# Kernel tuning notes

Hardware: AMD Instinct MI355X
Metric: run time of the kernel (lower is better)

## Reference

```python
import jax, jax.numpy as jnp
import numpy as np
import math

DIM = 768
HEADS = 12
HEAD_DIM = DIM // HEADS


def setup_inputs() -> dict:
    key = jax.random.key(0)
    ks = jax.random.split(key, 9)
    s = 1.0 / math.sqrt(DIM)
    x = jax.random.normal(ks[0], (8, 4096, DIM), dtype=jnp.float32)
    Wq = jax.random.normal(ks[1], (DIM, DIM), dtype=jnp.float32) * s
    bq = jnp.zeros((DIM,), dtype=jnp.float32)
    Wk = jax.random.normal(ks[2], (DIM, DIM), dtype=jnp.float32) * s
    bk = jnp.zeros((DIM,), dtype=jnp.float32)
    Wv = jax.random.normal(ks[3], (DIM, DIM), dtype=jnp.float32) * s
    bv = jnp.zeros((DIM,), dtype=jnp.float32)
    Wp = jax.random.normal(ks[4], (DIM, DIM), dtype=jnp.float32) * s
    bp = jnp.zeros((DIM,), dtype=jnp.float32)
    return {"x": x, "Wq": Wq, "bq": bq, "Wk": Wk, "bk": bk,
            "Wv": Wv, "bv": bv, "Wp": Wp, "bp": bp}


def reference(x, Wq, bq, Wk, bk, Wv, bv, Wp, bp):
    B, N, C = x.shape
    H, D = HEADS, HEAD_DIM
    # torch Linear: y = x @ W.T + b
    q = (x @ Wq.T + bq).reshape(B, N, H, D).transpose(0, 2, 1, 3)  # [B,H,N,D]
    k = (x @ Wk.T + bk).reshape(B, N, H, D).transpose(0, 2, 1, 3)
    v = (x @ Wv.T + bv).reshape(B, N, H, D).transpose(0, 2, 1, 3)
    q = jax.nn.softmax(q, axis=-1)   # softmax over head_dim
    k = jax.nn.softmax(k, axis=-2)   # softmax over sequence
    kv = jnp.einsum('bhnd,bhne->bhde', k, v) / math.sqrt(D)  # [B,H,D,D]
    out = jnp.einsum('bhnd,bhde->bhne', q, kv)               # [B,H,N,D]
    out = out.transpose(0, 2, 1, 3).reshape(B, N, C)
    return out @ Wp.T + bp
```

## Files before the change

kernel.cpp:

```cpp
#include <hip/hip_runtime.h>
#include <hip/hip_bf16.h>


#define AS1 __attribute__((address_space(1)))
#define AS3 __attribute__((address_space(3)))

typedef __attribute__((ext_vector_type(8))) short    s16x8;
typedef __attribute__((ext_vector_type(4))) float    f32x4;
typedef __attribute__((ext_vector_type(8))) _Float16 f16x8;
typedef __attribute__((ext_vector_type(4))) unsigned short u16x4;

__device__ __forceinline__ unsigned short f2bf(float f) {
  union { float f; unsigned u; } v; v.f = f;
  unsigned r = v.u + 0x7FFFu + ((v.u >> 16) & 1u);
  return (unsigned short)(r >> 16);
}

__global__ __launch_bounds__(256) void prep(const float* __restrict__ x,
                                            const float* __restrict__ Wq, const float* __restrict__ Wk,
                                            const float* __restrict__ Wv,
                                            const float* __restrict__ bq, const float* __restrict__ bk,
                                            const float* __restrict__ bv,
                                            unsigned short* __restrict__ x_bf,
                                            unsigned short* __restrict__ wqkv_bf,
                                            float* __restrict__ bqkv) {
  const int XB = 2304;
  if ((int)blockIdx.x >= XB) {
    int j = (blockIdx.x - XB) * 256 + threadIdx.x;
    if (j < 768) bqkv[j] = bq[j];
    else if (j < 1536) bqkv[j] = bk[j - 768];
    else if (j < 2304) bqkv[j] = bv[j - 1536];
    return;
  }
  const int n8x = 3145728, n8w = 73728;
  const int stride = XB * 256;
  for (int i = blockIdx.x * 256 + threadIdx.x; i < n8x + 3 * n8w; i += stride) {
    const float* s; unsigned short* d;
    if (i < n8x) { s = x + (size_t)i * 8; d = x_bf + (size_t)i * 8; }
    else {
      int wi = i - n8x, w = wi / n8w, off = wi - w * n8w;
      const float* ws_ = (w == 0) ? Wq : (w == 1) ? Wk : Wv;
      s = ws_ + (size_t)off * 8; d = wqkv_bf + (size_t)wi * 8;
    }
    f32x4 a = ((const f32x4*)s)[0], b = ((const f32x4*)s)[1];
    u16x4 lo, hi;
    lo[0] = f2bf(a[0]); lo[1] = f2bf(a[1]); lo[2] = f2bf(a[2]); lo[3] = f2bf(a[3]);
    hi[0] = f2bf(b[0]); hi[1] = f2bf(b[1]); hi[2] = f2bf(b[2]); hi[3] = f2bf(b[3]);
    ((u16x4*)d)[0] = lo; ((u16x4*)d)[1] = hi;
  }
}

template <int MODE>
__global__ __launch_bounds__(256, 3) void gemm128(const unsigned short* __restrict__ A,
                                                  const unsigned short* __restrict__ Bm,
                                                  const float* __restrict__ bias,
                                                  void* out0, void* out1, void* out2,
                                                  int N, int K, int nb, int batchedB) {
  __shared__ unsigned short As[128 * 64];
  __shared__ unsigned short Bs[128 * 64];
  const int tid = threadIdx.x, lane = tid & 63, wid = tid >> 6;
  const int wm = wid >> 1, wn = wid & 1;
  const int cpx = gridDim.x >> 3;
  const int logical = (blockIdx.x & 7) * cpx + (blockIdx.x >> 3);
  const int m0 = (logical / nb) * 128, n0 = (logical % nb) * 128;
  const unsigned short* Bp = Bm + (batchedB ? ((size_t)(m0 >> 12) * 589824) : 0);

  f32x4 acc[4][4] = {};
  const int srcc8 = ((tid & 7) ^ ((tid >> 3) & 7)) * 8;
  const int r15 = lane & 15, hi8 = (lane >> 4) * 8, sw = (lane & 7) * 8;

  const int nt = K >> 6;
  for (int t = 0; t < nt; ++t) {
    const int k0 = t << 6;
#pragma unroll
    for (int j = 0; j < 4; ++j) {
      int row = j * 32 + (tid >> 3);
      __builtin_amdgcn_global_load_lds(
          (const AS1 void*)(A + (size_t)(m0 + row) * K + k0 + srcc8),
          (AS3 void*)(&As[row * 64 + (tid & 7) * 8]), 16, 0, 0);
      __builtin_amdgcn_global_load_lds(
          (const AS1 void*)(Bp + (size_t)(n0 + row) * K + k0 + srcc8),
          (AS3 void*)(&Bs[row * 64 + (tid & 7) * 8]), 16, 0, 0);
    }
    __syncthreads();
#pragma unroll
    for (int kk = 0; kk < 2; ++kk) {
      s16x8 af[4], bf[4];
#pragma unroll
      for (int i = 0; i < 4; ++i)
        af[i] = *(const s16x8*)(As + (wm * 64 + i * 16 + r15) * 64 + ((kk * 32 + hi8) ^ sw));
#pragma unroll
      for (int j = 0; j < 4; ++j)
        bf[j] = *(const s16x8*)(Bs + (wn * 64 + j * 16 + r15) * 64 + ((kk * 32 + hi8) ^ sw));
#pragma unroll
      for (int i = 0; i < 4; ++i)
#pragma unroll
        for (int j = 0; j < 4; ++j)
          acc[i][j] = __builtin_amdgcn_mfma_f32_16x16x32_bf16(af[i], bf[j], acc[i][j], 0, 0, 0);
    }
    __syncthreads();
  }

  const int g = lane >> 4, c15 = lane & 15;
  float bj[4];
#pragma unroll
  for (int j = 0; j < 4; ++j) bj[j] = bias[n0 + wn * 64 + j * 16 + c15];

  if (MODE == 0) {
    float* out = (float*)out0;
#pragma unroll
    for (int mi = 0; mi < 4; ++mi)
#pragma unroll
      for (int j = 0; j < 4; ++j) {
        int gr = m0 + wm * 64 + mi * 16 + g * 4;
        int gc = n0 + wn * 64 + j * 16 + c15;
#pragma unroll
        for (int r = 0; r < 4; ++r)
          out[(size_t)(gr + r) * N + gc] = acc[mi][j][r] + bj[j];
      }
  } else {
    if (n0 < 768) {
      unsigned short* qsm = (unsigned short*)out0;
      const int cbase = n0 + wn * 64;
#pragma unroll
      for (int mi = 0; mi < 4; ++mi) {
#pragma unroll
        for (int r = 0; r < 4; ++r) {
          int gr = m0 + wm * 64 + mi * 16 + g * 4 + r;
          float v[4];
#pragma unroll
          for (int j = 0; j < 4; ++j) v[j] = acc[mi][j][r] + bj[j];
          float mx = fmaxf(fmaxf(v[0], v[1]), fmaxf(v[2], v[3]));
#pragma unroll
          for (int st = 1; st < 16; st <<= 1) mx = fmaxf(mx, __shfl_xor(mx, st));
          float p[4], sm = 0.f;
#pragma unroll
          for (int j = 0; j < 4; ++j) { p[j] = __expf(v[j] - mx); sm += p[j]; }
#pragma unroll
          for (int st = 1; st < 16; st <<= 1) sm += __shfl_xor(sm, st);
          float inv = 1.0f / sm;
#pragma unroll
          for (int j = 0; j < 4; ++j)
            qsm[(size_t)gr * 768 + cbase + j * 16 + c15] = f2bf(p[j] * inv);
        }
      }
    } else {
      _Float16* dst = (n0 < 1536) ? (_Float16*)out1 : (_Float16*)out2;
      const int cbase = (n0 < 1536 ? n0 - 768 : n0 - 1536) + wn * 64;
#pragma unroll
      for (int mi = 0; mi < 4; ++mi)
#pragma unroll
        for (int j = 0; j < 4; ++j) {
          int gr = m0 + wm * 64 + mi * 16 + g * 4;
          int cc = cbase + j * 16 + c15;
#pragma unroll
          for (int r = 0; r < 4; ++r)
            dst[(size_t)(gr + r) * 768 + cc] = (_Float16)(acc[mi][j][r] + bj[j]);
        }
    }
  }
}

__global__ __launch_bounds__(256) void kv_partial(const _Float16* __restrict__ kh,
                                                  const _Float16* __restrict__ vh,
                                                  float* __restrict__ kv_part,
                                                  float* __restrict__ z_part) {
  const int bh = blockIdx.x, b = bh / 12, h = bh % 12;
  const int split = blockIdx.y;
  __shared__ float ek_s[64][68];
  __shared__ float v_s[64][68];
  __shared__ float zred[4][64];
  const int t = threadIdx.x;
  const int d0 = (t >> 4) * 4, e0 = (t & 15) * 4;
  const int zd = t & 63, zq = t >> 6;
  float acc[4][4] = {};
  float zp = 0.f;
  const size_t base = (size_t)b * 4096 * 768 + h * 64;

  for (int nc = 0; nc < 8; ++nc) {
    int n0 = split * 512 + nc * 64;
#pragma unroll
    for (int j = 0; j < 2; ++j) {
      int vi = t + j * 256;
      int row = vi >> 3, c8 = (vi & 7) * 8;
      size_t gp = base + (size_t)(n0 + row) * 768 + c8;
      f16x8 k8 = *(const f16x8*)(kh + gp);
      f16x8 v8 = *(const f16x8*)(vh + gp);
      f32x4 e0v, e1v, v0v, v1v;
#pragma unroll
      for (int u = 0; u < 4; ++u) {
        e0v[u] = __expf((float)k8[u]); e1v[u] = __expf((float)k8[4 + u]);
        v0v[u] = (float)v8[u];         v1v[u] = (float)v8[4 + u];
      }
      *(f32x4*)&ek_s[row][c8] = e0v; *(f32x4*)&ek_s[row][c8 + 4] = e1v;
      *(f32x4*)&v_s[row][c8]  = v0v; *(f32x4*)&v_s[row][c8 + 4]  = v1v;
    }
    __syncthreads();
#pragma unroll 4
    for (int r = 0; r < 16; ++r) zp += ek_s[zq * 16 + r][zd];
#pragma unroll 8
    for (int n = 0; n < 64; ++n) {
      f32x4 ekv = *(const f32x4*)&ek_s[n][d0];
      f32x4 vv  = *(const f32x4*)&v_s[n][e0];
#pragma unroll
      for (int i = 0; i < 4; ++i)
#pragma unroll
        for (int j = 0; j < 4; ++j)
          acc[i][j] += ekv[i] * vv[j];
    }
    __syncthreads();
  }
  float* kvp = kv_part + ((size_t)split * 96 + bh) * 4096;
#pragma unroll
  for (int i = 0; i < 4; ++i)
#pragma unroll
    for (int j = 0; j < 4; ++j)
      kvp[(d0 + i) * 64 + e0 + j] = acc[i][j];
  zred[zq][zd] = zp;
  __syncthreads();
  if (t < 64)
    z_part[((size_t)split * 96 + bh) * 64 + t] =
        zred[0][t] + zred[1][t] + zred[2][t] + zred[3][t];
}

__global__ __launch_bounds__(256) void weff_build(const float* __restrict__ kv_part,
                                                  const float* __restrict__ z_part,
                                                  const float* __restrict__ Wp,
                                                  unsigned short* __restrict__ weffT) {
  const int c0 = blockIdx.x * 64, h = blockIdx.y, b = blockIdx.z;
  const int bh = b * 12 + h;
  __shared__ float kvn[64][65];
  __shared__ float zs[64];
  const int t = threadIdx.x;
  if (t < 64) {
    float s = 0.f;
#pragma unroll
    for (int sp = 0; sp < 8; ++sp) s += z_part[((size_t)sp * 96 + bh) * 64 + t];
    zs[t] = s * 8.0f;
  }
  __syncthreads();
#pragma unroll
  for (int i = 0; i < 16; ++i) {
    int idx = t + i * 256;
    int d = idx >> 6;
    float s = 0.f;
#pragma unroll
    for (int sp = 0; sp < 8; ++sp) s += kv_part[((size_t)sp * 96 + bh) * 4096 + idx];
    kvn[d][idx & 63] = s / zs[d];
  }
  __syncthreads();
  const int c = c0 + (t >> 2);
  const int d0 = (t & 3) * 16;
  const float* wrow = Wp + (size_t)c * 768 + h * 64;
  float acc[16] = {};
#pragma unroll 8
  for (int e = 0; e < 64; ++e) {
    float w = wrow[e];
#pragma unroll
    for (int dd = 0; dd < 16; ++dd) acc[dd] += w * kvn[d0 + dd][e];
  }
  unsigned short* orow = weffT + (size_t)b * 589824 + (size_t)c * 768 + h * 64 + d0;
#pragma unroll
  for (int dd = 0; dd < 16; ++dd) orow[dd] = f2bf(acc[dd]);
}

extern "C" void kernel_launch(void* const* d_in, const int* in_sizes, int n_in,
                              void* d_out, int out_size, void* d_ws, size_t ws_size,
                              hipStream_t stream) {
  const float* x  = (const float*)d_in[0];
  const float* Wq = (const float*)d_in[1];
  const float* bq = (const float*)d_in[2];
  const float* Wk = (const float*)d_in[3];
  const float* bk = (const float*)d_in[4];
  const float* Wv = (const float*)d_in[5];
  const float* bv = (const float*)d_in[6];
  const float* Wp = (const float*)d_in[7];
  const float* bp = (const float*)d_in[8];

  const size_t MT = 32768;
  const size_t XE = MT * 768;
  const size_t WE = 768 * 768;

  unsigned short* x_bf    = (unsigned short*)d_ws;
  unsigned short* wqkv_bf = x_bf + XE;
  unsigned short* q_sm    = wqkv_bf + 3 * WE;
  _Float16* k_h = (_Float16*)(q_sm + XE);
  _Float16* v_h = k_h + XE;
  unsigned short* weffT = (unsigned short*)(v_h + XE);
  float* bqkv    = (float*)(weffT + 8 * WE);
  float* kv_part = bqkv + 2304;
  float* z_part  = kv_part + (size_t)8 * 96 * 4096;

  prep<<<2313, 256, 0, stream>>>(x, Wq, Wk, Wv, bq, bk, bv, x_bf, wqkv_bf, bqkv);

  gemm128<1><<<4608, 256, 0, stream>>>(x_bf, wqkv_bf, bqkv, q_sm, k_h, v_h, 2304, 768, 18, 0);

  kv_partial<<<dim3(96, 8), 256, 0, stream>>>(k_h, v_h, kv_part, z_part);
  weff_build<<<dim3(12, 12, 8), 256, 0, stream>>>(kv_part, z_part, Wp, weffT);

  gemm128<0><<<1536, 256, 0, stream>>>(q_sm, weffT, bp, d_out, nullptr, nullptr, 768, 768, 6, 1);
}
```

Measured before the change: 319.5 us.

## Split kv_partial sequence rows across waves with 8x8 per-thread tiles and LDS reduction

Each wave now takes a quarter of each 64-row chunk, and every thread accumulates an 8x8 kv tile instead of a 4x4 tile over all rows. This halves the LDS loads per FMA and uses vector FMAs. The four partial tiles are then combined in LDS with a tree reduction before wave 0 writes the result. The trade-off is more accumulator registers, which may lower occupancy, plus three extra barriers and LDS traffic at the end.

Result: no change. 319.0 us (-0.1%).

```diff
diff --git a/kernel.cpp b/kernel.cpp
--- a/kernel.cpp
+++ b/kernel.cpp
@@ -170,10 +170,10 @@
   __shared__ float ek_s[64][68];
   __shared__ float v_s[64][68];
   __shared__ float zred[4][64];
-  const int t = threadIdx.x;
-  const int d0 = (t >> 4) * 4, e0 = (t & 15) * 4;
+  const int t = threadIdx.x, lane = t & 63, w = t >> 6;
+  const int d0 = (lane & 7) * 8, e0 = (lane >> 3) * 8;
   const int zd = t & 63, zq = t >> 6;
-  float acc[4][4] = {};
+  f32x4 acc4[8][2] = {};
   float zp = 0.f;
   const size_t base = (size_t)b * 4096 * 768 + h * 64;
 
@@ -198,24 +198,55 @@
     __syncthreads();
 #pragma unroll 4
     for (int r = 0; r < 16; ++r) zp += ek_s[zq * 16 + r][zd];
-#pragma unroll 8
-    for (int n = 0; n < 64; ++n) {
-      f32x4 ekv = *(const f32x4*)&ek_s[n][d0];
-      f32x4 vv  = *(const f32x4*)&v_s[n][e0];
-#pragma unroll
-      for (int i = 0; i < 4; ++i)
-#pragma unroll
-        for (int j = 0; j < 4; ++j)
-          acc[i][j] += ekv[i] * vv[j];
+#pragma unroll 4
+    for (int r = 0; r < 16; ++r) {
+      int n = w * 16 + r;
+      f32x4 ea = *(const f32x4*)&ek_s[n][d0];
+      f32x4 eb = *(const f32x4*)&ek_s[n][d0 + 4];
+      f32x4 va = *(const f32x4*)&v_s[n][e0];
+      f32x4 vb = *(const f32x4*)&v_s[n][e0 + 4];
+#pragma unroll
+      for (int i = 0; i < 4; ++i) {
+        acc4[i][0] += va * ea[i];     acc4[i][1] += vb * ea[i];
+        acc4[4 + i][0] += va * eb[i]; acc4[4 + i][1] += vb * eb[i];
+      }
     }
     __syncthreads();
   }
-  float* kvp = kv_part + ((size_t)split * 96 + bh) * 4096;
-#pragma unroll
-  for (int i = 0; i < 4; ++i)
-#pragma unroll
-    for (int j = 0; j < 4; ++j)
-      kvp[(d0 + i) * 64 + e0 + j] = acc[i][j];
+
+  float* redA = &ek_s[0][0];
+  float* redB = &v_s[0][0];
+  auto wr_red = [&](float* red) {
+#pragma unroll
+    for (int i = 0; i < 8; ++i) {
+      *(f32x4*)&red[(d0 + i) * 68 + e0]     = acc4[i][0];
+      *(f32x4*)&red[(d0 + i) * 68 + e0 + 4] = acc4[i][1];
+    }
+  };
+  auto add_red = [&](const float* red) {
+#pragma unroll
+    for (int i = 0; i < 8; ++i) {
+      acc4[i][0] += *(const f32x4*)&red[(d0 + i) * 68 + e0];
+      acc4[i][1] += *(const f32x4*)&red[(d0 + i) * 68 + e0 + 4];
+    }
+  };
+  if (w == 1) wr_red(redA);
+  if (w == 3) wr_red(redB);
+  __syncthreads();
+  if (w == 0) add_red(redA);
+  if (w == 2) add_red(redB);
+  __syncthreads();
+  if (w == 2) wr_red(redA);
+  __syncthreads();
+  if (w == 0) {
+    add_red(redA);
+    float* kvp = kv_part + ((size_t)split * 96 + bh) * 4096;
+#pragma unroll
+    for (int i = 0; i < 8; ++i) {
+      *(f32x4*)&kvp[(d0 + i) * 64 + e0]     = acc4[i][0];
+      *(f32x4*)&kvp[(d0 + i) * 64 + e0 + 4] = acc4[i][1];
+    }
+  }
   zred[zq][zd] = zp;
   __syncthreads();
   if (t < 64)
```
